# Kernel optimization log

Measured on AMD Instinct MI355X. Metric: run time of the kernel, lower is better.

Reference implementation:

```python
import jax, jax.numpy as jnp
import numpy as np

N = 50000
E = 800000
DIN = 64   # input_dim
DE = 32    # edge_dim
HID = 32   # hidden_dim (per-head channels for layers 0,1)
DOUT = 64  # output_dim


def _lin_init(key, fan_in, fan_out):
    return jax.random.normal(key, (fan_in, fan_out), dtype=jnp.float32) / np.sqrt(fan_in)


def setup_inputs() -> dict:
    key = jax.random.key(0)
    ks = list(jax.random.split(key, 64))
    inp = {}
    inp["x"] = jax.random.normal(ks[0], (N, DIN), dtype=jnp.float32)
    inp["edge_attr"] = jax.random.normal(ks[1], (E, DE), dtype=jnp.float32)
    inp["edge_index"] = jax.random.randint(ks[2], (2, E), 0, N, dtype=jnp.int32)
    # layer dims: (in_dim, heads, per-head out C, skip_out)
    dims = [(DIN, 2, HID, 2 * HID), (2 * HID, 2, HID, 2 * HID), (2 * HID, 1, DOUT, DOUT)]
    ki = 3
    for l, (din, H, C, dskip) in enumerate(dims):
        HC = H * C
        inp[f"Wq{l}"] = _lin_init(ks[ki], din, HC); ki += 1
        inp[f"bq{l}"] = jnp.zeros((HC,), jnp.float32)
        inp[f"Wk{l}"] = _lin_init(ks[ki], din, HC); ki += 1
        inp[f"bk{l}"] = jnp.zeros((HC,), jnp.float32)
        inp[f"Wv{l}"] = _lin_init(ks[ki], din, HC); ki += 1
        inp[f"bv{l}"] = jnp.zeros((HC,), jnp.float32)
        inp[f"We{l}"] = _lin_init(ks[ki], DE, HC); ki += 1  # lin_edge, bias=False in PyG
        inp[f"Ws{l}"] = _lin_init(ks[ki], din, dskip); ki += 1  # lin_skip (root weight)
        inp[f"bs{l}"] = jnp.zeros((dskip,), jnp.float32)
    inp["prelu_a"] = jnp.asarray(0.25, dtype=jnp.float32)
    return inp


def _transformer_conv(x, src, dst, eattr, Wq, bq, Wk, bk, Wv, bv, We, Ws, bs, H, C, concat):
    n = x.shape[0]
    q = (x @ Wq + bq).reshape(n, H, C)
    k = (x @ Wk + bk).reshape(n, H, C)
    v = (x @ Wv + bv).reshape(n, H, C)
    e = (eattr @ We).reshape(-1, H, C)          # [E,H,C] edge embedding
    kj = k[src] + e                              # key of source + edge
    alpha = jnp.sum(q[dst] * kj, axis=-1) / jnp.sqrt(jnp.float32(C))  # [E,H]
    # scatter softmax over incoming edges per destination node
    m = jax.ops.segment_max(alpha, dst, num_segments=n)
    a = jnp.exp(alpha - m[dst])
    s = jax.ops.segment_sum(a, dst, num_segments=n)
    a = a / (s[dst] + 1e-16)
    vj = v[src] + e                              # value of source + edge
    out = jax.ops.segment_sum(a[..., None] * vj, dst, num_segments=n)  # [N,H,C]
    out = out.reshape(n, H * C) if concat else jnp.mean(out, axis=1)
    return out + x @ Ws + bs                     # root/skip connection


def reference(x, edge_attr, edge_index,
              Wq0, bq0, Wk0, bk0, Wv0, bv0, We0, Ws0, bs0,
              Wq1, bq1, Wk1, bk1, Wv1, bv1, We1, Ws1, bs1,
              Wq2, bq2, Wk2, bk2, Wv2, bv2, We2, Ws2, bs2,
              prelu_a):
    src, dst = edge_index[0], edge_index[1]
    h = _transformer_conv(x, src, dst, edge_attr, Wq0, bq0, Wk0, bk0, Wv0, bv0, We0, Ws0, bs0, 2, HID, True)
    h = jnp.where(h >= 0, h, prelu_a * h)
    h = _transformer_conv(h, src, dst, edge_attr, Wq1, bq1, Wk1, bk1, Wv1, bv1, We1, Ws1, bs1, 2, HID, True)
    h = jnp.where(h >= 0, h, prelu_a * h)
    h = _transformer_conv(h, src, dst, edge_attr, Wq2, bq2, Wk2, bk2, Wv2, bv2, We2, Ws2, bs2, 1, DOUT, False)
    return h
```

## Files before the change

kernel.cpp:

```cpp
#include <hip/hip_runtime.h>
#include <hip/hip_bf16.h>


#define NDIM 64
#define LOG2E 1.4426950408889634f

static __device__ __forceinline__ unsigned short f2bu(float f) {
  __hip_bfloat16 b = __float2bfloat16(f);
  return *reinterpret_cast<unsigned short*>(&b);
}

__global__ void k_count(const int* __restrict__ ei, int* __restrict__ cnt, int E) {
  int i = blockIdx.x * blockDim.x + threadIdx.x;
  if (i < E) atomicAdd(&cnt[ei[E + i]], 1);
}

__global__ __launch_bounds__(256) void k_scanA(const int* __restrict__ cnt,
                                               int* __restrict__ tpre,
                                               int* __restrict__ btot, int n) {
  int t = threadIdx.x, b = blockIdx.x;
  int base = (b * 256 + t) * 4;
  int s = 0;
  if (base + 3 < n) {
    int4 v = *(const int4*)(cnt + base);
    s = v.x + v.y + v.z + v.w;
  } else if (base < n) {
    for (int k = 0; k < 4 && base + k < n; ++k) s += cnt[base + k];
  }
  __shared__ int ps[256];
  ps[t] = s;
  __syncthreads();
  for (int off = 1; off < 256; off <<= 1) {
    int v = (t >= off) ? ps[t - off] : 0;
    __syncthreads();
    ps[t] += v;
    __syncthreads();
  }
  tpre[b * 256 + t] = ps[t] - s;
  if (t == 255) btot[b] = ps[255];
}

__global__ void k_scanB(int* __restrict__ btot, int nb, int* __restrict__ rowptr, int n) {
  int lane = threadIdx.x & 63;
  int v = (lane < nb) ? btot[lane] : 0;
  int inc = v;
#pragma unroll
  for (int off = 1; off < 64; off <<= 1) {
    int u = __shfl_up(inc, off);
    if (lane >= off) inc += u;
  }
  if (lane < nb) btot[lane] = inc - v;
  if (lane == 63) rowptr[n] = inc;
}

__global__ __launch_bounds__(256) void k_scanC(const int* __restrict__ cnt,
                                               const int* __restrict__ tpre,
                                               const int* __restrict__ btot,
                                               int* __restrict__ rowptr, int n) {
  int t = threadIdx.x, b = blockIdx.x;
  int base = (b * 256 + t) * 4;
  if (base >= n) return;
  int p = btot[b] + tpre[b * 256 + t];
  if (base + 3 < n) {
    int4 v = *(const int4*)(cnt + base);
    rowptr[base] = p; p += v.x;
    rowptr[base + 1] = p; p += v.y;
    rowptr[base + 2] = p; p += v.z;
    rowptr[base + 3] = p;
  } else {
    for (int k = 0; k < 4 && base + k < n; ++k) { rowptr[base + k] = p; p += cnt[base + k]; }
  }
}

__global__ void k_scatter(const int* __restrict__ ei, int* __restrict__ fill,
                          const int* __restrict__ rowptr,
                          int* __restrict__ srcs, int* __restrict__ perm, int E) {
  int i = blockIdx.x * blockDim.x + threadIdx.x;
  if (i < E) {
    int d = ei[E + i];
    int pos = rowptr[d] + atomicAdd(&fill[d], 1);
    srcs[pos] = ei[i];
    perm[pos] = i;
  }
}

__global__ __launch_bounds__(256) void k_permea(const int* __restrict__ perm,
                                                const float4* __restrict__ ea,
                                                ushort4* __restrict__ eab, int E) {
  int tid = blockIdx.x * 256 + threadIdx.x;
  int pos = tid >> 3, t = tid & 7;
  if (pos >= E) return;
  int i = perm[pos];
  float4 v = ea[(size_t)i * 8 + t];
  ushort4 u;
  u.x = f2bu(v.x); u.y = f2bu(v.y); u.z = f2bu(v.z); u.w = f2bu(v.w);
  eab[(size_t)pos * 8 + t] = u;
}

template <int H>
__global__ __launch_bounds__(256) void k_node(
    const float* __restrict__ h,
    const float* __restrict__ Wq, const float* __restrict__ bq,
    const float* __restrict__ Wk, const float* __restrict__ bk,
    const float* __restrict__ Wv, const float* __restrict__ bv,
    const float* __restrict__ Ws, const float* __restrict__ bs,
    const float* __restrict__ We,
    float* __restrict__ qs, unsigned int* __restrict__ kvw,
    float* __restrict__ qe, int N)
{
  __shared__ float hL[64][64];
  __shared__ float qL[64][64];
  __shared__ float WeT[2048];
  int t = threadIdx.x;
  int nb = blockIdx.x * 64;
  int m = t >> 6, c = t & 63;
  const float* W = (m == 0) ? Wq : (m == 1) ? Wk : (m == 2) ? Wv : Ws;
  const float* B = (m == 0) ? bq : (m == 1) ? bk : (m == 2) ? bv : bs;
  float w[64];
#pragma unroll
  for (int d = 0; d < 64; ++d) w[d] = W[d * 64 + c];
  float bias = B[c];
#pragma unroll
  for (int f = t; f < 2048; f += 256) WeT[(f >> 5) * 32 + (f & 31)] = We[(f & 31) * 64 + (f >> 5)];
  int nmax = N - nb; if (nmax > 64) nmax = 64;
#pragma unroll
  for (int j = 0; j < 16; ++j) {
    int flat = j * 256 + t;
    int ni = flat >> 6;
    if (ni < nmax) hL[ni][flat & 63] = h[(size_t)(nb + ni) * 64 + (flat & 63)];
  }
  __syncthreads();
  for (int i = 0; i < nmax; ++i) {
    float acc = bias;
    const float4* hr = (const float4*)&hL[i][0];
#pragma unroll
    for (int d4 = 0; d4 < 16; ++d4) {
      float4 hv = hr[d4];
      acc = fmaf(hv.x, w[4 * d4 + 0], acc);
      acc = fmaf(hv.y, w[4 * d4 + 1], acc);
      acc = fmaf(hv.z, w[4 * d4 + 2], acc);
      acc = fmaf(hv.w, w[4 * d4 + 3], acc);
    }
    size_t n = (size_t)(nb + i);
    if (m == 0)      { qs[n * 128 + c] = acc; qL[i][c] = acc; }
    else if (m == 3) qs[n * 128 + 64 + c] = acc;
    else ((unsigned short*)kvw)[(n * 64 + c) * 2 + (m == 2 ? 1 : 0)] = f2bu(acc);
  }
  __syncthreads();
  int slot = t & 63, ibase = (t >> 6) * 16;
  int half = slot >> 5, d = slot & 31;
  float wreg[32];
#pragma unroll
  for (int cc = 0; cc < 32; ++cc) wreg[cc] = WeT[(half * 32 + cc) * 32 + d];
  for (int ii = 0; ii < 16; ++ii) {
    int i = ibase + ii;
    if (i >= nmax) break;
    float acc = 0.f;
    const float4* qr = (const float4*)&qL[i][half * 32];
#pragma unroll
    for (int c4 = 0; c4 < 8; ++c4) {
      float4 qv = qr[c4];
      acc = fmaf(qv.x, wreg[4 * c4 + 0], acc);
      acc = fmaf(qv.y, wreg[4 * c4 + 1], acc);
      acc = fmaf(qv.z, wreg[4 * c4 + 2], acc);
      acc = fmaf(qv.w, wreg[4 * c4 + 3], acc);
    }
    size_t n = (size_t)(nb + i);
    if (H == 2) {
      qe[n * 64 + slot] = acc;
    } else {
      float tot = acc + __shfl_xor(acc, 32);
      qe[n * 64 + slot] = (slot < 32) ? tot : 0.f;
    }
  }
}

template <int H, bool LAST>
__global__ __launch_bounds__(256) void k_attn(
    const float* __restrict__ qs,
    const unsigned int* __restrict__ kvw,
    const float* __restrict__ qe,
    const __hip_bfloat16* __restrict__ eab,
    const float* __restrict__ We,
    const int* __restrict__ rowptr,
    const int* __restrict__ srcs,
    const float* __restrict__ prelu_a,
    float* __restrict__ hout, int N)
{
  int wave = threadIdx.x >> 6;
  int lane = threadIdx.x & 63;
  int wgid = blockIdx.x * 4 + wave;
  const int W = gridDim.x * 4;
  const float pmul = ((H == 2) ? 0.17677669529663687f : 0.125f) * LOG2E;
  const int RW = (H == 2) ? 32 : 64;
  int el = lane & 31;

  float wecol[32];
#pragma unroll
  for (int d = 0; d < 32; ++d) wecol[d] = We[d * 64 + lane];
  float pa = LAST ? 0.f : prelu_a[0];

  for (int rep = 0; rep < 4; ++rep) {
    int dst = wgid + rep * W;
    if (dst >= N) break;

    float q_c = qs[(size_t)dst * 128 + lane] * pmul;
    float qe_c = qe[(size_t)dst * 64 + lane] * pmul;

    float m = -1e30f, s = 0.f, accv = 0.f, acce = 0.f;
    int jb = rowptr[dst], je = rowptr[dst + 1];
    int j = jb;
    for (; j + 4 <= je; j += 4) {
      int s0 = srcs[j], s1 = srcs[j + 1], s2 = srcs[j + 2], s3 = srcs[j + 3];
      unsigned int w0 = kvw[(size_t)s0 * 64 + lane];
      unsigned int w1 = kvw[(size_t)s1 * 64 + lane];
      unsigned int w2 = kvw[(size_t)s2 * 64 + lane];
      unsigned int w3 = kvw[(size_t)s3 * 64 + lane];
      float a0 = __uint_as_float(((unsigned int)*(const unsigned short*)&eab[(size_t)(j + 0) * 32 + el]) << 16);
      float a1 = __uint_as_float(((unsigned int)*(const unsigned short*)&eab[(size_t)(j + 1) * 32 + el]) << 16);
      float a2 = __uint_as_float(((unsigned int)*(const unsigned short*)&eab[(size_t)(j + 2) * 32 + el]) << 16);
      float a3 = __uint_as_float(((unsigned int)*(const unsigned short*)&eab[(size_t)(j + 3) * 32 + el]) << 16);
      float k0 = __uint_as_float(w0 << 16), v0 = __uint_as_float(w0 & 0xFFFF0000u);
      float k1 = __uint_as_float(w1 << 16), v1 = __uint_as_float(w1 & 0xFFFF0000u);
      float k2 = __uint_as_float(w2 << 16), v2 = __uint_as_float(w2 & 0xFFFF0000u);
      float k3 = __uint_as_float(w3 << 16), v3 = __uint_as_float(w3 & 0xFFFF0000u);
      float x0 = fmaf(q_c, k0, qe_c * a0);
      float x1 = fmaf(q_c, k1, qe_c * a1);
      float x2 = fmaf(q_c, k2, qe_c * a2);
      float x3 = fmaf(q_c, k3, qe_c * a3);
#pragma unroll
      for (int off = 1; off < RW; off <<= 1) {
        x0 += __shfl_xor(x0, off);
        x1 += __shfl_xor(x1, off);
        x2 += __shfl_xor(x2, off);
        x3 += __shfl_xor(x3, off);
      }
      float mx = fmaxf(fmaxf(x0, x1), fmaxf(x2, x3));
      if (__any(mx > m + 16.f)) {
        float mn = fmaxf(m, mx);
        float sc = exp2f(m - mn);
        s *= sc; accv *= sc; acce *= sc;
        m = mn;
      }
      float q0 = exp2f(x0 - m), q1 = exp2f(x1 - m);
      float q2 = exp2f(x2 - m), q3 = exp2f(x3 - m);
      s += (q0 + q1) + (q2 + q3);
      accv += fmaf(q0, v0, q1 * v1) + fmaf(q2, v2, q3 * v3);
      acce += fmaf(q0, a0, q1 * a1) + fmaf(q2, a2, q3 * a3);
    }
    for (; j < je; ++j) {
      int s0 = srcs[j];
      unsigned int w0 = kvw[(size_t)s0 * 64 + lane];
      float k0 = __uint_as_float(w0 << 16), v0 = __uint_as_float(w0 & 0xFFFF0000u);
      float a0 = __uint_as_float(((unsigned int)*(const unsigned short*)&eab[(size_t)j * 32 + el]) << 16);
      float x0 = fmaf(q_c, k0, qe_c * a0);
#pragma unroll
      for (int off = 1; off < RW; off <<= 1) x0 += __shfl_xor(x0, off);
      float mn = fmaxf(m, x0);
      float sc = exp2f(m - mn);
      float q0 = exp2f(x0 - mn);
      s = s * sc + q0;
      accv = accv * sc + q0 * v0;
      acce = acce * sc + q0 * a0;
      m = mn;
    }

    int base = (H == 2) ? (lane & 32) : 0;
    float sum = accv;
#pragma unroll
    for (int d = 0; d < 32; ++d) {
      float aead = __shfl(acce, base + d);
      sum = fmaf(aead, wecol[d], sum);
    }
    float out = sum / (s + 1e-16f);
    out += qs[(size_t)dst * 128 + 64 + lane];
    if (!LAST) out = (out >= 0.f) ? out : pa * out;
    hout[(size_t)dst * 64 + lane] = out;
  }
}

extern "C" void kernel_launch(void* const* d_in, const int* in_sizes, int n_in,
                              void* d_out, int out_size, void* d_ws, size_t ws_size,
                              hipStream_t stream) {
  const int N = in_sizes[0] / NDIM;
  const int E = in_sizes[2] / 2;

  const float* x  = (const float*)d_in[0];
  const float* ea = (const float*)d_in[1];
  const int* ei   = (const int*)d_in[2];
  const float* prelu = (const float*)d_in[30];
  auto W = [&](int l, int k) { return (const float*)d_in[3 + 9 * l + k]; };

  const int nbScan = (N + 1023) / 1024;

  char* p = (char*)d_ws;
  auto alloc = [&](size_t bytes) { char* r = p; p += (bytes + 255) & ~(size_t)255; return r; };
  float* h             = (float*)alloc((size_t)N * 64 * 4);
  float* qs            = (float*)alloc((size_t)N * 128 * 4);
  unsigned int* kvw    = (unsigned int*)alloc((size_t)N * 64 * 4);
  float* qe            = (float*)alloc((size_t)N * 64 * 4);
  __hip_bfloat16* eab  = (__hip_bfloat16*)alloc((size_t)E * 32 * 2);
  int* rowptr          = (int*)alloc((size_t)(N + 1) * 4);
  int* cntfill         = (int*)alloc((size_t)2 * N * 4);
  int* cnt = cntfill;
  int* fill = cntfill + N;
  int* srcs            = (int*)alloc((size_t)E * 4);
  int* perm            = (int*)alloc((size_t)E * 4);
  int* tpre            = (int*)alloc((size_t)nbScan * 256 * 4);
  int* btot            = (int*)alloc((size_t)64 * 4);
  (void)ws_size; (void)n_in; (void)out_size;

  hipMemsetAsync(cntfill, 0, (size_t)2 * N * 4, stream);

  k_count<<<(E + 255) / 256, 256, 0, stream>>>(ei, cnt, E);
  k_scanA<<<nbScan, 256, 0, stream>>>(cnt, tpre, btot, N);
  k_scanB<<<1, 64, 0, stream>>>(btot, nbScan, rowptr, N);
  k_scanC<<<nbScan, 256, 0, stream>>>(cnt, tpre, btot, rowptr, N);
  k_scatter<<<(E + 255) / 256, 256, 0, stream>>>(ei, fill, rowptr, srcs, perm, E);
  k_permea<<<(E * 8 + 255) / 256, 256, 0, stream>>>(perm, (const float4*)ea, (ushort4*)eab, E);

  const int attnBlocks = (N + 15) / 16;
  for (int l = 0; l < 3; ++l) {
    const float* hin = (l == 0) ? x : h;
    if (l < 2) {
      k_node<2><<<(N + 63) / 64, 256, 0, stream>>>(
          hin, W(l, 0), W(l, 1), W(l, 2), W(l, 3), W(l, 4), W(l, 5), W(l, 7), W(l, 8),
          W(l, 6), qs, kvw, qe, N);
      k_attn<2, false><<<attnBlocks, 256, 0, stream>>>(
          qs, kvw, qe, eab, W(l, 6), rowptr, srcs, prelu, h, N);
    } else {
      k_node<1><<<(N + 63) / 64, 256, 0, stream>>>(
          hin, W(l, 0), W(l, 1), W(l, 2), W(l, 3), W(l, 4), W(l, 5), W(l, 7), W(l, 8),
          W(l, 6), qs, kvw, qe, N);
      k_attn<1, true><<<attnBlocks, 256, 0, stream>>>(
          qs, kvw, qe, eab, W(l, 6), rowptr, srcs, prelu, (float*)d_out, N);
    }
  }
}
```

Baseline: 784.2 us.

## Drop edge-attr permutation pass; gather bf16 edge attrs by original index

```diff
diff --git a/kernel.cpp b/kernel.cpp
--- a/kernel.cpp
+++ b/kernel.cpp
@@ -3,16 +3,23 @@
 
 
 #define NDIM 64
-#define LOG2E 1.4426950408889634f
 
 static __device__ __forceinline__ unsigned short f2bu(float f) {
   __hip_bfloat16 b = __float2bfloat16(f);
   return *reinterpret_cast<unsigned short*>(&b);
 }
 
-__global__ void k_count(const int* __restrict__ ei, int* __restrict__ cnt, int E) {
-  int i = blockIdx.x * blockDim.x + threadIdx.x;
-  if (i < E) atomicAdd(&cnt[ei[E + i]], 1);
+__global__ __launch_bounds__(256) void k_count_cvt(
+    const int* __restrict__ ei, int* __restrict__ cnt,
+    const float4* __restrict__ ea, ushort4* __restrict__ eab, int E) {
+  int tid = blockIdx.x * 256 + threadIdx.x;
+  int pos = tid >> 3, t = tid & 7;
+  if (pos >= E) return;
+  float4 v = ea[(size_t)pos * 8 + t];
+  ushort4 u;
+  u.x = f2bu(v.x); u.y = f2bu(v.y); u.z = f2bu(v.z); u.w = f2bu(v.w);
+  eab[(size_t)pos * 8 + t] = u;
+  if (t == 0) atomicAdd(&cnt[ei[E + pos]], 1);
 }
 
 __global__ __launch_bounds__(256) void k_scanA(const int* __restrict__ cnt,
@@ -73,28 +80,13 @@
 }
 
 __global__ void k_scatter(const int* __restrict__ ei, int* __restrict__ fill,
-                          const int* __restrict__ rowptr,
-                          int* __restrict__ srcs, int* __restrict__ perm, int E) {
+                          const int* __restrict__ rowptr, int2* __restrict__ pairs, int E) {
   int i = blockIdx.x * blockDim.x + threadIdx.x;
   if (i < E) {
     int d = ei[E + i];
     int pos = rowptr[d] + atomicAdd(&fill[d], 1);
-    srcs[pos] = ei[i];
-    perm[pos] = i;
-  }
-}
-
-__global__ __launch_bounds__(256) void k_permea(const int* __restrict__ perm,
-                                                const float4* __restrict__ ea,
-                                                ushort4* __restrict__ eab, int E) {
-  int tid = blockIdx.x * 256 + threadIdx.x;
-  int pos = tid >> 3, t = tid & 7;
-  if (pos >= E) return;
-  int i = perm[pos];
-  float4 v = ea[(size_t)i * 8 + t];
-  ushort4 u;
-  u.x = f2bu(v.x); u.y = f2bu(v.y); u.z = f2bu(v.z); u.w = f2bu(v.w);
-  eab[(size_t)pos * 8 + t] = u;
+    pairs[pos] = make_int2(ei[i], i);
+  }
 }
 
 template <int H>
@@ -183,100 +175,95 @@
     const __hip_bfloat16* __restrict__ eab,
     const float* __restrict__ We,
     const int* __restrict__ rowptr,
-    const int* __restrict__ srcs,
+    const int2* __restrict__ pairs,
     const float* __restrict__ prelu_a,
     float* __restrict__ hout, int N)
 {
   int wave = threadIdx.x >> 6;
   int lane = threadIdx.x & 63;
-  int wgid = blockIdx.x * 4 + wave;
-  const int W = gridDim.x * 4;
-  const float pmul = ((H == 2) ? 0.17677669529663687f : 0.125f) * LOG2E;
+  int dst = blockIdx.x * 4 + wave;
+  if (dst >= N) return;
+  const float rsC = (H == 2) ? 0.17677669529663687f : 0.125f;
   const int RW = (H == 2) ? 32 : 64;
   int el = lane & 31;
 
+  float q_c = qs[(size_t)dst * 128 + lane];
+  float qe_c = qe[(size_t)dst * 64 + lane];
+
+  float m = -1e30f, s = 0.f, accv = 0.f, acce = 0.f;
+  int jb = rowptr[dst], je = rowptr[dst + 1];
+  int j = jb;
+  for (; j + 4 <= je; j += 4) {
+    int2 p0 = pairs[j], p1 = pairs[j + 1], p2 = pairs[j + 2], p3 = pairs[j + 3];
+    unsigned int w0 = kvw[(size_t)p0.x * 64 + lane];
+    unsigned int w1 = kvw[(size_t)p1.x * 64 + lane];
+    unsigned int w2 = kvw[(size_t)p2.x * 64 + lane];
+    unsigned int w3 = kvw[(size_t)p3.x * 64 + lane];
+    float a0 = __uint_as_float(((unsigned int)*(const unsigned short*)&eab[(size_t)p0.y * 32 + el]) << 16);
+    float a1 = __uint_as_float(((unsigned int)*(const unsigned short*)&eab[(size_t)p1.y * 32 + el]) << 16);
+    float a2 = __uint_as_float(((unsigned int)*(const unsigned short*)&eab[(size_t)p2.y * 32 + el]) << 16);
+    float a3 = __uint_as_float(((unsigned int)*(const unsigned short*)&eab[(size_t)p3.y * 32 + el]) << 16);
+    float k0 = __uint_as_float(w0 << 16), v0 = __uint_as_float(w0 & 0xFFFF0000u);
+    float k1 = __uint_as_float(w1 << 16), v1 = __uint_as_float(w1 & 0xFFFF0000u);
+    float k2 = __uint_as_float(w2 << 16), v2 = __uint_as_float(w2 & 0xFFFF0000u);
+    float k3 = __uint_as_float(w3 << 16), v3 = __uint_as_float(w3 & 0xFFFF0000u);
+    float x0 = fmaf(q_c, k0, qe_c * a0);
+    float x1 = fmaf(q_c, k1, qe_c * a1);
+    float x2 = fmaf(q_c, k2, qe_c * a2);
+    float x3 = fmaf(q_c, k3, qe_c * a3);
+#pragma unroll
+    for (int off = 1; off < RW; off <<= 1) {
+      x0 += __shfl_xor(x0, off);
+      x1 += __shfl_xor(x1, off);
+      x2 += __shfl_xor(x2, off);
+      x3 += __shfl_xor(x3, off);
+    }
+    x0 *= rsC; x1 *= rsC; x2 *= rsC; x3 *= rsC;
+    float mx = fmaxf(fmaxf(x0, x1), fmaxf(x2, x3));
+    float mn = fmaxf(m, mx);
+    float sc = __expf(m - mn);
+    float q0 = __expf(x0 - mn), q1 = __expf(x1 - mn);
+    float q2 = __expf(x2 - mn), q3 = __expf(x3 - mn);
+    s = s * sc + ((q0 + q1) + (q2 + q3));
+    accv = accv * sc + (fmaf(q0, v0, q1 * v1) + fmaf(q2, v2, q3 * v3));
+    acce = acce * sc + (fmaf(q0, a0, q1 * a1) + fmaf(q2, a2, q3 * a3));
+    m = mn;
+  }
+  for (; j < je; ++j) {
+    int2 p0 = pairs[j];
+    unsigned int w0 = kvw[(size_t)p0.x * 64 + lane];
+    float k0 = __uint_as_float(w0 << 16), v0 = __uint_as_float(w0 & 0xFFFF0000u);
+    float a0 = __uint_as_float(((unsigned int)*(const unsigned short*)&eab[(size_t)p0.y * 32 + el]) << 16);
+    float x0 = fmaf(q_c, k0, qe_c * a0);
+#pragma unroll
+    for (int off = 1; off < RW; off <<= 1) x0 += __shfl_xor(x0, off);
+    x0 *= rsC;
+    float mn = fmaxf(m, x0);
+    float sc = __expf(m - mn);
+    float q0 = __expf(x0 - mn);
+    s = s * sc + q0;
+    accv = accv * sc + q0 * v0;
+    acce = acce * sc + q0 * a0;
+    m = mn;
+  }
+
   float wecol[32];
 #pragma unroll
   for (int d = 0; d < 32; ++d) wecol[d] = We[d * 64 + lane];
-  float pa = LAST ? 0.f : prelu_a[0];
-
-  for (int rep = 0; rep < 4; ++rep) {
-    int dst = wgid + rep * W;
-    if (dst >= N) break;
-
-    float q_c = qs[(size_t)dst * 128 + lane] * pmul;
-    float qe_c = qe[(size_t)dst * 64 + lane] * pmul;
-
-    float m = -1e30f, s = 0.f, accv = 0.f, acce = 0.f;
-    int jb = rowptr[dst], je = rowptr[dst + 1];
-    int j = jb;
-    for (; j + 4 <= je; j += 4) {
-      int s0 = srcs[j], s1 = srcs[j + 1], s2 = srcs[j + 2], s3 = srcs[j + 3];
-      unsigned int w0 = kvw[(size_t)s0 * 64 + lane];
-      unsigned int w1 = kvw[(size_t)s1 * 64 + lane];
-      unsigned int w2 = kvw[(size_t)s2 * 64 + lane];
-      unsigned int w3 = kvw[(size_t)s3 * 64 + lane];
-      float a0 = __uint_as_float(((unsigned int)*(const unsigned short*)&eab[(size_t)(j + 0) * 32 + el]) << 16);
-      float a1 = __uint_as_float(((unsigned int)*(const unsigned short*)&eab[(size_t)(j + 1) * 32 + el]) << 16);
-      float a2 = __uint_as_float(((unsigned int)*(const unsigned short*)&eab[(size_t)(j + 2) * 32 + el]) << 16);
-      float a3 = __uint_as_float(((unsigned int)*(const unsigned short*)&eab[(size_t)(j + 3) * 32 + el]) << 16);
-      float k0 = __uint_as_float(w0 << 16), v0 = __uint_as_float(w0 & 0xFFFF0000u);
-      float k1 = __uint_as_float(w1 << 16), v1 = __uint_as_float(w1 & 0xFFFF0000u);
-      float k2 = __uint_as_float(w2 << 16), v2 = __uint_as_float(w2 & 0xFFFF0000u);
-      float k3 = __uint_as_float(w3 << 16), v3 = __uint_as_float(w3 & 0xFFFF0000u);
-      float x0 = fmaf(q_c, k0, qe_c * a0);
-      float x1 = fmaf(q_c, k1, qe_c * a1);
-      float x2 = fmaf(q_c, k2, qe_c * a2);
-      float x3 = fmaf(q_c, k3, qe_c * a3);
-#pragma unroll
-      for (int off = 1; off < RW; off <<= 1) {
-        x0 += __shfl_xor(x0, off);
-        x1 += __shfl_xor(x1, off);
-        x2 += __shfl_xor(x2, off);
-        x3 += __shfl_xor(x3, off);
-      }
-      float mx = fmaxf(fmaxf(x0, x1), fmaxf(x2, x3));
-      if (__any(mx > m + 16.f)) {
-        float mn = fmaxf(m, mx);
-        float sc = exp2f(m - mn);
-        s *= sc; accv *= sc; acce *= sc;
-        m = mn;
-      }
-      float q0 = exp2f(x0 - m), q1 = exp2f(x1 - m);
-      float q2 = exp2f(x2 - m), q3 = exp2f(x3 - m);
-      s += (q0 + q1) + (q2 + q3);
-      accv += fmaf(q0, v0, q1 * v1) + fmaf(q2, v2, q3 * v3);
-      acce += fmaf(q0, a0, q1 * a1) + fmaf(q2, a2, q3 * a3);
-    }
-    for (; j < je; ++j) {
-      int s0 = srcs[j];
-      unsigned int w0 = kvw[(size_t)s0 * 64 + lane];
-      float k0 = __uint_as_float(w0 << 16), v0 = __uint_as_float(w0 & 0xFFFF0000u);
-      float a0 = __uint_as_float(((unsigned int)*(const unsigned short*)&eab[(size_t)j * 32 + el]) << 16);
-      float x0 = fmaf(q_c, k0, qe_c * a0);
-#pragma unroll
-      for (int off = 1; off < RW; off <<= 1) x0 += __shfl_xor(x0, off);
-      float mn = fmaxf(m, x0);
-      float sc = exp2f(m - mn);
-      float q0 = exp2f(x0 - mn);
-      s = s * sc + q0;
-      accv = accv * sc + q0 * v0;
-      acce = acce * sc + q0 * a0;
-      m = mn;
-    }
-
-    int base = (H == 2) ? (lane & 32) : 0;
-    float sum = accv;
-#pragma unroll
-    for (int d = 0; d < 32; ++d) {
-      float aead = __shfl(acce, base + d);
-      sum = fmaf(aead, wecol[d], sum);
-    }
-    float out = sum / (s + 1e-16f);
-    out += qs[(size_t)dst * 128 + 64 + lane];
-    if (!LAST) out = (out >= 0.f) ? out : pa * out;
-    hout[(size_t)dst * 64 + lane] = out;
-  }
+  int base = (H == 2) ? (lane & 32) : 0;
+  float sum = accv;
+#pragma unroll
+  for (int d = 0; d < 32; ++d) {
+    float aead = __shfl(acce, base + d);
+    sum = fmaf(aead, wecol[d], sum);
+  }
+  float out = sum / (s + 1e-16f);
+  out += qs[(size_t)dst * 128 + 64 + lane];
+  if (!LAST) {
+    float a = prelu_a[0];
+    out = (out >= 0.f) ? out : a * out;
+  }
+  hout[(size_t)dst * 64 + lane] = out;
 }
 
 extern "C" void kernel_launch(void* const* d_in, const int* in_sizes, int n_in,
@@ -304,36 +291,34 @@
   int* cntfill         = (int*)alloc((size_t)2 * N * 4);
   int* cnt = cntfill;
   int* fill = cntfill + N;
-  int* srcs            = (int*)alloc((size_t)E * 4);
-  int* perm            = (int*)alloc((size_t)E * 4);
+  int2* pairs          = (int2*)alloc((size_t)E * 8);
   int* tpre            = (int*)alloc((size_t)nbScan * 256 * 4);
   int* btot            = (int*)alloc((size_t)64 * 4);
   (void)ws_size; (void)n_in; (void)out_size;
 
   hipMemsetAsync(cntfill, 0, (size_t)2 * N * 4, stream);
 
-  k_count<<<(E + 255) / 256, 256, 0, stream>>>(ei, cnt, E);
+  k_count_cvt<<<(E * 8 + 255) / 256, 256, 0, stream>>>(ei, cnt, (const float4*)ea,
+                                                       (ushort4*)eab, E);
   k_scanA<<<nbScan, 256, 0, stream>>>(cnt, tpre, btot, N);
   k_scanB<<<1, 64, 0, stream>>>(btot, nbScan, rowptr, N);
   k_scanC<<<nbScan, 256, 0, stream>>>(cnt, tpre, btot, rowptr, N);
-  k_scatter<<<(E + 255) / 256, 256, 0, stream>>>(ei, fill, rowptr, srcs, perm, E);
-  k_permea<<<(E * 8 + 255) / 256, 256, 0, stream>>>(perm, (const float4*)ea, (ushort4*)eab, E);
-
-  const int attnBlocks = (N + 15) / 16;
+  k_scatter<<<(E + 255) / 256, 256, 0, stream>>>(ei, fill, rowptr, pairs, E);
+
   for (int l = 0; l < 3; ++l) {
     const float* hin = (l == 0) ? x : h;
     if (l < 2) {
       k_node<2><<<(N + 63) / 64, 256, 0, stream>>>(
           hin, W(l, 0), W(l, 1), W(l, 2), W(l, 3), W(l, 4), W(l, 5), W(l, 7), W(l, 8),
           W(l, 6), qs, kvw, qe, N);
-      k_attn<2, false><<<attnBlocks, 256, 0, stream>>>(
-          qs, kvw, qe, eab, W(l, 6), rowptr, srcs, prelu, h, N);
+      k_attn<2, false><<<(N + 3) / 4, 256, 0, stream>>>(
+          qs, kvw, qe, eab, W(l, 6), rowptr, pairs, prelu, h, N);
     } else {
       k_node<1><<<(N + 63) / 64, 256, 0, stream>>>(
           hin, W(l, 0), W(l, 1), W(l, 2), W(l, 3), W(l, 4), W(l, 5), W(l, 7), W(l, 8),
           W(l, 6), qs, kvw, qe, N);
-      k_attn<1, true><<<attnBlocks, 256, 0, stream>>>(
-          qs, kvw, qe, eab, W(l, 6), rowptr, srcs, prelu, (float*)d_out, N);
-    }
-  }
-}
+      k_attn<1, true><<<(N + 3) / 4, 256, 0, stream>>>(
+          qs, kvw, qe, eab, W(l, 6), rowptr, pairs, prelu, (float*)d_out, N);
+    }
+  }
+}
```

Measured after the change: 683.9 us. 1.15x faster.
